# Kernel optimization log

Hardware: AMD Instinct MI355X
Metric: run time of the kernel (lower is better)

## Reference

```python
import jax, jax.numpy as jnp
import numpy as np

N, C_IN, C_OUT, J = 4096, 256, 256, 2
ATT_SLICE = C_OUT * J  # 512
DENSITY = 0.01
NEG_FILL = -1e20


def _sparse_lap(key, n):
    k1, k2 = jax.random.split(key)
    vals = jax.random.normal(k1, (n, n), dtype=jnp.float32)
    mask = jax.random.uniform(k2, (n, n)) < DENSITY
    return vals * mask + jnp.eye(n, dtype=jnp.float32)


def setup_inputs() -> dict:
    key = jax.random.key(0)
    ks = jax.random.split(key, 12)
    s = 0.05
    return {
        "x": jax.random.normal(ks[0], (N, C_IN), dtype=jnp.float32),
        "Lup": _sparse_lap(ks[1], N),
        "Ld": _sparse_lap(ks[2], N),
        "P": _sparse_lap(ks[3], N),
        "Wirr_w": jax.random.normal(ks[4], (J, C_OUT, C_IN), dtype=jnp.float32) * s,
        "Wirr_b": jax.random.normal(ks[5], (J, C_OUT), dtype=jnp.float32) * s,
        "Wsol_w": jax.random.normal(ks[6], (J, C_OUT, C_IN), dtype=jnp.float32) * s,
        "Wsol_b": jax.random.normal(ks[7], (J, C_OUT), dtype=jnp.float32) * s,
        "Whar_w": jax.random.normal(ks[8], (C_OUT, C_IN), dtype=jnp.float32) * s,
        "Whar_b": jax.random.normal(ks[9], (C_OUT,), dtype=jnp.float32) * s,
        "att_irr": jax.random.normal(ks[10], (2 * ATT_SLICE, 1), dtype=jnp.float32) * s,
        "att_sol": jax.random.normal(ks[11], (2 * ATT_SLICE, 1), dtype=jnp.float32) * s,
    }


def _branch(x, L, Ww, Wb, att):
    # x_cat = concat_j(Linear_j(x)) : [N, J*C_OUT]
    x_cat = (jnp.einsum('nc,jdc->njd', x, Ww) + Wb).reshape(x.shape[0], -1)
    src = x_cat @ att[:ATT_SLICE, :]   # [N,1]
    dst = x_cat @ att[ATT_SLICE:, :]   # [N,1]
    E = jax.nn.leaky_relu(src + dst.T, negative_slope=0.01)  # [N,N]
    E = jnp.where(L != 0, E, NEG_FILL)
    alpha = jax.nn.softmax(E, axis=-1)
    z = (alpha @ x) @ Ww[0].T + Wb[0]
    for p in range(1, J):  # Laplacian-power diffusion
        alpha = alpha @ L
        z = z + (alpha @ x) @ Ww[p].T + Wb[p]
    return z


def reference(x, Lup, Ld, P, Wirr_w, Wirr_b, Wsol_w, Wsol_b, Whar_w, Whar_b, att_irr, att_sol):
    z_i = _branch(x, Ld, Wirr_w, Wirr_b, att_irr)
    z_s = _branch(x, Lup, Wsol_w, Wsol_b, att_sol)
    z_har = (P @ x) @ Whar_w.T + Whar_b
    return z_i + z_s + z_har
```

## Files before the change

### kernel.cpp

```cpp
#include <hip/hip_runtime.h>

#define NROW 4096
#define CH   256
#define MAXNNZ 128

typedef short  short8  __attribute__((ext_vector_type(8)));
typedef unsigned short ushort8 __attribute__((ext_vector_type(8)));
typedef float  f32x4   __attribute__((ext_vector_type(4)));

__device__ inline unsigned short f2bf(float f) {
  unsigned u = __float_as_uint(f);
  return (unsigned short)((u + 0x7fffu + ((u >> 16) & 1u)) >> 16);
}
__device__ inline float bf2f(unsigned short h) {
  return __uint_as_float((unsigned)h << 16);
}
__device__ inline int mbcnt64(unsigned long long m, int base) {
  int t = __builtin_amdgcn_mbcnt_lo((unsigned)m, (unsigned)base);
  return __builtin_amdgcn_mbcnt_hi((unsigned)(m >> 32), t);
}

__global__ void cvt_all(const float* __restrict__ x, const float* __restrict__ Wi,
                        const float* __restrict__ Ws, const float* __restrict__ Wh,
                        unsigned short* __restrict__ xbf, unsigned short* __restrict__ Bbf) {
  int i = blockIdx.x * 256 + threadIdx.x;
  const float* src; unsigned short* dst; int o;
  if (i < 262144)        { src = x;  dst = xbf;          o = i; }
  else if (i < 294912)   { src = Wi; dst = Bbf;          o = i - 262144; }
  else if (i < 327680)   { src = Ws; dst = Bbf + 131072; o = i - 294912; }
  else                   { src = Wh; dst = Bbf + 262144; o = i - 327680; }
  float4 v = ((const float4*)src)[o];
  ushort4 u;
  u.x = f2bf(v.x); u.y = f2bf(v.y); u.z = f2bf(v.z); u.w = f2bf(v.w);
  ((ushort4*)dst)[o] = u;
}

__global__ __launch_bounds__(256) void scan_gemm(
    const float* __restrict__ L0, const float* __restrict__ L1,
    const float* __restrict__ L2, int* __restrict__ idx,
    float* __restrict__ val, int* __restrict__ cnt,
    const unsigned short* __restrict__ A, const unsigned short* __restrict__ Bt,
    unsigned short* __restrict__ Y) {
  __shared__ __align__(16) union {
    struct { unsigned short sA[64 * 128]; unsigned short sB[64 * 128]; } g;
    struct { int sj[4][MAXNNZ]; float sv[4][MAXNNZ]; int scnt[4]; } c;
  } u;
  const int bid = blockIdx.x, tid = threadIdx.x;
  const bool is_gemm = (bid < 12800) && (bid % 10 == 9);

  if (is_gemm) {
    const int gid = bid / 10;
    const int m0 = (gid & 63) * 64, n0 = (gid >> 6) * 64;
    const int wid = tid >> 6, lane = tid & 63;
    const int wr = wid >> 1, wc = wid & 1, lr = lane & 15, kg = lane >> 4;
    f32x4 acc[2][2] = {};
#pragma unroll
    for (int kh = 0; kh < 2; ++kh) {
      for (int c = 0; c < 4; ++c) {
        int chunk = c * 256 + tid;
        int r  = chunk >> 4;
        int cb = (chunk & 15) * 16;
        int cbs = cb ^ ((r & 7) << 4);
        ushort8 va = *(const ushort8*)((const char*)A  + (size_t)(m0 + r) * 512 + kh * 256 + cb);
        *(ushort8*)((char*)u.g.sA + r * 256 + cbs) = va;
        ushort8 vb = *(const ushort8*)((const char*)Bt + (size_t)(n0 + r) * 512 + kh * 256 + cb);
        *(ushort8*)((char*)u.g.sB + r * 256 + cbs) = vb;
      }
      __syncthreads();
#pragma unroll
      for (int ks = 0; ks < 4; ++ks) {
        int kb = ks * 64 + kg * 16;
        short8 a0, a1, b0, b1;
        { int r = wr * 32 + lr;      a0 = *(const short8*)((const char*)u.g.sA + r * 256 + (kb ^ ((r & 7) << 4))); }
        { int r = wr * 32 + 16 + lr; a1 = *(const short8*)((const char*)u.g.sA + r * 256 + (kb ^ ((r & 7) << 4))); }
        { int r = wc * 32 + lr;      b0 = *(const short8*)((const char*)u.g.sB + r * 256 + (kb ^ ((r & 7) << 4))); }
        { int r = wc * 32 + 16 + lr; b1 = *(const short8*)((const char*)u.g.sB + r * 256 + (kb ^ ((r & 7) << 4))); }
        acc[0][0] = __builtin_amdgcn_mfma_f32_16x16x32_bf16(a0, b0, acc[0][0], 0, 0, 0);
        acc[0][1] = __builtin_amdgcn_mfma_f32_16x16x32_bf16(a0, b1, acc[0][1], 0, 0, 0);
        acc[1][0] = __builtin_amdgcn_mfma_f32_16x16x32_bf16(a1, b0, acc[1][0], 0, 0, 0);
        acc[1][1] = __builtin_amdgcn_mfma_f32_16x16x32_bf16(a1, b1, acc[1][1], 0, 0, 0);
      }
      __syncthreads();
    }
#pragma unroll
    for (int mi = 0; mi < 2; ++mi)
#pragma unroll
      for (int ni = 0; ni < 2; ++ni) {
        int col = n0 + wc * 32 + ni * 16 + lr;
#pragma unroll
        for (int r4 = 0; r4 < 4; ++r4) {
          int row = m0 + wr * 32 + mi * 16 + kg * 4 + r4;
          Y[(size_t)row * 1280 + col] = f2bf(acc[mi][ni][r4]);
        }
      }
  } else {
    const int cid = bid - ((bid < 12800) ? (bid + 1) / 10 : 1280);
    const int mat = cid >> 12, row = cid & 4095;
    const float* L = (mat == 0) ? L0 : (mat == 1) ? L1 : L2;
    const int wi = tid >> 6, lane = tid & 63;
    const float4* Lseg = (const float4*)(L + (size_t)row * NROW) + wi * 256;

    float4 v0 = Lseg[lane], v1 = Lseg[64 + lane], v2 = Lseg[128 + lane], v3 = Lseg[192 + lane];

    int base = 0;
    float4 vv[4] = {v0, v1, v2, v3};
#pragma unroll
    for (int k = 0; k < 4; ++k) {
      float4 q = vv[k];
      bool n0_ = q.x != 0.f, n1_ = q.y != 0.f, n2_ = q.z != 0.f, n3_ = q.w != 0.f;
      unsigned long long b0 = __ballot(n0_), b1 = __ballot(n1_);
      unsigned long long b2 = __ballot(n2_), b3 = __ballot(n3_);
      int off = mbcnt64(b3, mbcnt64(b2, mbcnt64(b1, mbcnt64(b0, base))));
      int col0 = wi * 1024 + k * 256 + lane * 4;
      if (n0_) { if (off < MAXNNZ) { u.c.sj[wi][off] = col0;     u.c.sv[wi][off] = q.x; } ++off; }
      if (n1_) { if (off < MAXNNZ) { u.c.sj[wi][off] = col0 + 1; u.c.sv[wi][off] = q.y; } ++off; }
      if (n2_) { if (off < MAXNNZ) { u.c.sj[wi][off] = col0 + 2; u.c.sv[wi][off] = q.z; } ++off; }
      if (n3_) { if (off < MAXNNZ) { u.c.sj[wi][off] = col0 + 3; u.c.sv[wi][off] = q.w; } ++off; }
      base += __popcll(b0) + __popcll(b1) + __popcll(b2) + __popcll(b3);
    }
    if (lane == 0) u.c.scnt[wi] = base < MAXNNZ ? base : MAXNNZ;
    __syncthreads();

    int c0 = u.c.scnt[0], c1 = u.c.scnt[1], c2 = u.c.scnt[2], c3 = u.c.scnt[3];
    int total = c0 + c1 + c2 + c3;
    if (total > MAXNNZ) total = MAXNNZ;
    size_t rbase = ((size_t)mat * NROW + row) * MAXNNZ;
    int t = tid;
    if (t < total) {
      int s, o;
      if      (t < c0)           { s = 0; o = t; }
      else if (t < c0 + c1)      { s = 1; o = t - c0; }
      else if (t < c0 + c1 + c2) { s = 2; o = t - c0 - c1; }
      else                       { s = 3; o = t - c0 - c1 - c2; }
      idx[rbase + t] = u.c.sj[s][o];
      val[rbase + t] = u.c.sv[s][o];
    }
    if (t == 0) cnt[mat * NROW + row] = total;
  }
}

__global__ __launch_bounds__(256) void spmm_sdv(
    const int* __restrict__ idx, const float* __restrict__ val,
    const int* __restrict__ cnt, const float* __restrict__ ai,
    const float* __restrict__ as_, const float* __restrict__ bi,
    const float* __restrict__ bs, unsigned short* __restrict__ Y,
    float* __restrict__ sdv) {
  int row = blockIdx.x, t = threadIdx.x, w = t >> 6, l = t & 63;
  __shared__ float satt[2048];
  __shared__ float red2[8];
  __shared__ float sbias[4];
  __shared__ int   sj0[MAXNNZ], sj1[MAXNNZ];
  __shared__ float sv0[MAXNNZ], sv1[MAXNNZ];
  __shared__ float part[4][256];

  for (int k = t; k < 1024; k += 256) { satt[k] = ai[k]; satt[1024 + k] = as_[k]; }
  {
    const float* av = (w & 2) ? as_ : ai;
    const float* bv = (w & 2) ? bs : bi;
    int off = (w & 1) * 512;
    float b = 0.f;
    for (int k = l; k < 512; k += 64) b += av[off + k] * bv[k];
    for (int o = 32; o; o >>= 1) b += __shfl_xor(b, o);
    if (l == 0) sbias[w] = b;
  }
  int n0 = cnt[row], n1 = cnt[NROW + row];
  if (t < n0) { sj0[t] = idx[(size_t)row * MAXNNZ + t];          sv0[t] = val[(size_t)row * MAXNNZ + t]; }
  if (t < n1) { sj1[t] = idx[((size_t)NROW + row) * MAXNNZ + t]; sv1[t] = val[((size_t)NROW + row) * MAXNNZ + t]; }
  ushort4 y4 = *(const ushort4*)(Y + (size_t)row * 1280 + 4 * t);
  __syncthreads();

  {
    int c0 = 4 * t;
    int aoff = (t < 128) ? 0 : 1024;
    int cc = c0 & 511;
    float sp = satt[aoff + cc]       * bf2f(y4.x) + satt[aoff + cc + 1]       * bf2f(y4.y)
             + satt[aoff + cc + 2]   * bf2f(y4.z) + satt[aoff + cc + 3]       * bf2f(y4.w);
    float dp = satt[aoff + 512 + cc] * bf2f(y4.x) + satt[aoff + 512 + cc + 1] * bf2f(y4.y)
             + satt[aoff + 512 + cc + 2] * bf2f(y4.z) + satt[aoff + 512 + cc + 3] * bf2f(y4.w);
    for (int o = 32; o; o >>= 1) { sp += __shfl_xor(sp, o); dp += __shfl_xor(dp, o); }
    if (l == 0) { red2[w * 2] = sp; red2[w * 2 + 1] = dp; }
  }

  float4 acc0 = {0.f, 0.f, 0.f, 0.f}, acc1 = {0.f, 0.f, 0.f, 0.f};
  for (int k = w; k < n0; k += 4) {
    ushort4 y = *(const ushort4*)(Y + (size_t)sj0[k] * 1280 + 256 + 4 * l);
    float a = sv0[k];
    acc0.x += a * bf2f(y.x); acc0.y += a * bf2f(y.y);
    acc0.z += a * bf2f(y.z); acc0.w += a * bf2f(y.w);
  }
  for (int k = w; k < n1; k += 4) {
    ushort4 y = *(const ushort4*)(Y + (size_t)sj1[k] * 1280 + 768 + 4 * l);
    float a = sv1[k];
    acc1.x += a * bf2f(y.x); acc1.y += a * bf2f(y.y);
    acc1.z += a * bf2f(y.z); acc1.w += a * bf2f(y.w);
  }
  ((float4*)part[w])[l] = acc0;
  __syncthreads();
  if (t == 0) {
    sdv[row]            = red2[0] + red2[2] + sbias[0];
    sdv[NROW + row]     = red2[1] + red2[3] + sbias[1];
    sdv[2 * NROW + row] = red2[4] + red2[6] + sbias[2];
    sdv[3 * NROW + row] = red2[5] + red2[7] + sbias[3];
  }
  if (t < 64) {
    unsigned short* yp = Y + (size_t)row * 1280 + 4 * t;
    ushort4 yb = *(const ushort4*)yp;
    ushort4 o;
    o.x = f2bf(bf2f(yb.x) + part[0][4 * t]     + part[1][4 * t]     + part[2][4 * t]     + part[3][4 * t]);
    o.y = f2bf(bf2f(yb.y) + part[0][4 * t + 1] + part[1][4 * t + 1] + part[2][4 * t + 1] + part[3][4 * t + 1]);
    o.z = f2bf(bf2f(yb.z) + part[0][4 * t + 2] + part[1][4 * t + 2] + part[2][4 * t + 2] + part[3][4 * t + 2]);
    o.w = f2bf(bf2f(yb.w) + part[0][4 * t + 3] + part[1][4 * t + 3] + part[2][4 * t + 3] + part[3][4 * t + 3]);
    *(ushort4*)yp = o;
  }
  __syncthreads();
  ((float4*)part[w])[l] = acc1;
  __syncthreads();
  if (t < 64) {
    unsigned short* yp = Y + (size_t)row * 1280 + 512 + 4 * t;
    ushort4 yb = *(const ushort4*)yp;
    ushort4 o;
    o.x = f2bf(bf2f(yb.x) + part[0][4 * t]     + part[1][4 * t]     + part[2][4 * t]     + part[3][4 * t]);
    o.y = f2bf(bf2f(yb.y) + part[0][4 * t + 1] + part[1][4 * t + 1] + part[2][4 * t + 1] + part[3][4 * t + 1]);
    o.z = f2bf(bf2f(yb.z) + part[0][4 * t + 2] + part[1][4 * t + 2] + part[2][4 * t + 2] + part[3][4 * t + 2]);
    o.w = f2bf(bf2f(yb.w) + part[0][4 * t + 3] + part[1][4 * t + 3] + part[2][4 * t + 3] + part[3][4 * t + 3]);
    *(ushort4*)yp = o;
  }
}

__global__ __launch_bounds__(256) void final_z(const int* __restrict__ idx,
                        const float* __restrict__ val, const int* __restrict__ cnt,
                        const float* __restrict__ sdv,
                        const unsigned short* __restrict__ Y,
                        const float* __restrict__ bi, const float* __restrict__ bs,
                        const float* __restrict__ bh, float* __restrict__ Z) {
  int row = blockIdx.x, t = threadIdx.x, w = t >> 6, l = t & 63;
  __shared__ float sa[MAXNNZ];
  __shared__ int   sj[MAXNNZ];
  __shared__ float red[4];
  __shared__ float part[4][256];
  float4 acc = {0.f, 0.f, 0.f, 0.f};

  for (int br = 0; br < 2; ++br) {
    size_t rbase = ((size_t)br * NROW + row) * MAXNNZ;
    int n = cnt[br * NROW + row];
    const float* srcv = sdv + (2 * br) * NROW;
    const float* dstv = sdv + (2 * br + 1) * NROW;
    float e = -1e30f;
    if (t < n) {
      int j = idx[rbase + t];
      sj[t] = j;
      float v = srcv[row] + dstv[j];
      e = v >= 0.f ? v : 0.01f * v;
    }
    float m = e;
    for (int o = 32; o; o >>= 1) m = fmaxf(m, __shfl_xor(m, o));
    if ((t & 63) == 0) red[t >> 6] = m;
    __syncthreads();
    m = fmaxf(fmaxf(red[0], red[1]), fmaxf(red[2], red[3]));
    __syncthreads();
    float p = (t < n) ? expf(e - m) : 0.f;
    float s = p;
    for (int o = 32; o; o >>= 1) s += __shfl_xor(s, o);
    if ((t & 63) == 0) red[t >> 6] = s;
    __syncthreads();
    s = red[0] + red[1] + red[2] + red[3];
    if (t < n) sa[t] = p / s;
    __syncthreads();
    int cd = br ? 512 : 0;
    for (int k = w; k < n; k += 4) {
      ushort4 y = *(const ushort4*)(Y + (size_t)sj[k] * 1280 + cd + 4 * l);
      float a = sa[k];
      acc.x += a * bf2f(y.x); acc.y += a * bf2f(y.y);
      acc.z += a * bf2f(y.z); acc.w += a * bf2f(y.w);
    }
    __syncthreads();
  }

  {
    size_t rbase = ((size_t)2 * NROW + row) * MAXNNZ;
    int n = cnt[2 * NROW + row];
    if (t < n) { sj[t] = idx[rbase + t]; sa[t] = val[rbase + t]; }
    __syncthreads();
    for (int k = w; k < n; k += 4) {
      ushort4 y = *(const ushort4*)(Y + (size_t)sj[k] * 1280 + 1024 + 4 * l);
      float a = sa[k];
      acc.x += a * bf2f(y.x); acc.y += a * bf2f(y.y);
      acc.z += a * bf2f(y.z); acc.w += a * bf2f(y.w);
    }
  }
  ((float4*)part[w])[l] = acc;
  __syncthreads();
  if (t < 64) {
    float4 r;
    int c = 4 * t;
    r.x = part[0][c]     + part[1][c]     + part[2][c]     + part[3][c]     + bi[c]     + bi[256 + c] + bs[c]     + bs[256 + c] + bh[c];
    r.y = part[0][c + 1] + part[1][c + 1] + part[2][c + 1] + part[3][c + 1] + bi[c + 1] + bi[257 + c] + bs[c + 1] + bs[257 + c] + bh[c + 1];
    r.z = part[0][c + 2] + part[1][c + 2] + part[2][c + 2] + part[3][c + 2] + bi[c + 2] + bi[258 + c] + bs[c + 2] + bs[258 + c] + bh[c + 2];
    r.w = part[0][c + 3] + part[1][c + 3] + part[2][c + 3] + part[3][c + 3] + bi[c + 3] + bi[259 + c] + bs[c + 3] + bs[259 + c] + bh[c + 3];
    *(float4*)(Z + (size_t)row * 256 + c) = r;
  }
}

extern "C" void kernel_launch(void* const* d_in, const int* in_sizes, int n_in,
                              void* d_out, int out_size, void* d_ws, size_t ws_size,
                              hipStream_t stream) {
  const float* x      = (const float*)d_in[0];
  const float* Lup    = (const float*)d_in[1];
  const float* Ld     = (const float*)d_in[2];
  const float* P      = (const float*)d_in[3];
  const float* Wirr_w = (const float*)d_in[4];
  const float* Wirr_b = (const float*)d_in[5];
  const float* Wsol_w = (const float*)d_in[6];
  const float* Wsol_b = (const float*)d_in[7];
  const float* Whar_w = (const float*)d_in[8];
  const float* Whar_b = (const float*)d_in[9];
  const float* att_i  = (const float*)d_in[10];
  const float* att_s  = (const float*)d_in[11];
  float* Z = (float*)d_out;

  char* w = (char*)d_ws;
  auto alloc = [&](size_t bytes) { void* p = (void*)w; w += (bytes + 255) & ~(size_t)255; return p; };

  int*   idx  = (int*)alloc((size_t)3 * NROW * MAXNNZ * 4);
  float* val  = (float*)alloc((size_t)3 * NROW * MAXNNZ * 4);
  int*   cnt  = (int*)alloc((size_t)3 * NROW * 4);
  float* sdv  = (float*)alloc(4 * NROW * 4);
  unsigned short* xbf = (unsigned short*)alloc((size_t)NROW * CH * 2);
  unsigned short* Bbf = (unsigned short*)alloc((size_t)1280 * CH * 2);
  unsigned short* Y   = (unsigned short*)alloc((size_t)NROW * 1280 * 2);

  cvt_all<<<(262144 + 32768 + 32768 + 16384) / 256, 256, 0, stream>>>(x, Wirr_w, Wsol_w, Whar_w, xbf, Bbf);

  scan_gemm<<<13568, 256, 0, stream>>>(Ld, Lup, P, idx, val, cnt, xbf, Bbf, Y);

  spmm_sdv<<<NROW, 256, 0, stream>>>(idx, val, cnt, att_i, att_s, Wirr_b, Wsol_b, Y, sdv);

  final_z<<<NROW, 256, 0, stream>>>(idx, val, cnt, sdv, Y, Wirr_b, Wsol_b, Whar_b, Z);
}
```

Measured before the change: 107.8 us.

## Move P-matrix scan into SpMM kernel to overlap with sparse gather work

The CSR compaction scan of the third dense matrix (P) moves out of the combined scan+GEMM kernel and into the SpMM/score kernel. Even blocks scan rows of P while odd blocks do the SpMM, sharing LDS through a union. The GEMM-interleave ratio in the first kernel is retuned to 1 in 7 to fit the smaller scan grid. The aim is to balance memory-bound dense scanning against the latency-bound gather SpMM so the two overlap, instead of leaving the SpMM kernel short of bandwidth-heavy work. The cost is a larger second grid and branch-divergent block roles.

Measured after the change: 122.7 us. 13.9% more time.

```diff
diff --git a/kernel.cpp b/kernel.cpp
--- a/kernel.cpp
+++ b/kernel.cpp
@@ -37,8 +37,7 @@
 
 __global__ __launch_bounds__(256) void scan_gemm(
     const float* __restrict__ L0, const float* __restrict__ L1,
-    const float* __restrict__ L2, int* __restrict__ idx,
-    float* __restrict__ val, int* __restrict__ cnt,
+    int* __restrict__ idx, float* __restrict__ val, int* __restrict__ cnt,
     const unsigned short* __restrict__ A, const unsigned short* __restrict__ Bt,
     unsigned short* __restrict__ Y) {
   __shared__ __align__(16) union {
@@ -46,10 +45,10 @@
     struct { int sj[4][MAXNNZ]; float sv[4][MAXNNZ]; int scnt[4]; } c;
   } u;
   const int bid = blockIdx.x, tid = threadIdx.x;
-  const bool is_gemm = (bid < 12800) && (bid % 10 == 9);
+  const bool is_gemm = (bid < 8960) && (bid % 7 == 6);
 
   if (is_gemm) {
-    const int gid = bid / 10;
+    const int gid = bid / 7;
     const int m0 = (gid & 63) * 64, n0 = (gid >> 6) * 64;
     const int wid = tid >> 6, lane = tid & 63;
     const int wr = wid >> 1, wc = wid & 1, lr = lane & 15, kg = lane >> 4;
@@ -94,9 +93,9 @@
         }
       }
   } else {
-    const int cid = bid - ((bid < 12800) ? (bid + 1) / 10 : 1280);
+    const int cid = (bid < 8960) ? (bid - (bid + 1) / 7) : (bid - 1280);
     const int mat = cid >> 12, row = cid & 4095;
-    const float* L = (mat == 0) ? L0 : (mat == 1) ? L1 : L2;
+    const float* L = (mat == 0) ? L0 : L1;
     const int wi = tid >> 6, lane = tid & 63;
     const float4* Lseg = (const float4*)(L + (size_t)row * NROW) + wi * 256;
 
@@ -139,91 +138,134 @@
   }
 }
 
-__global__ __launch_bounds__(256) void spmm_sdv(
-    const int* __restrict__ idx, const float* __restrict__ val,
-    const int* __restrict__ cnt, const float* __restrict__ ai,
-    const float* __restrict__ as_, const float* __restrict__ bi,
-    const float* __restrict__ bs, unsigned short* __restrict__ Y,
-    float* __restrict__ sdv) {
-  int row = blockIdx.x, t = threadIdx.x, w = t >> 6, l = t & 63;
-  __shared__ float satt[2048];
-  __shared__ float red2[8];
-  __shared__ float sbias[4];
-  __shared__ int   sj0[MAXNNZ], sj1[MAXNNZ];
-  __shared__ float sv0[MAXNNZ], sv1[MAXNNZ];
-  __shared__ float part[4][256];
-
-  for (int k = t; k < 1024; k += 256) { satt[k] = ai[k]; satt[1024 + k] = as_[k]; }
-  {
-    const float* av = (w & 2) ? as_ : ai;
-    const float* bv = (w & 2) ? bs : bi;
-    int off = (w & 1) * 512;
-    float b = 0.f;
-    for (int k = l; k < 512; k += 64) b += av[off + k] * bv[k];
-    for (int o = 32; o; o >>= 1) b += __shfl_xor(b, o);
-    if (l == 0) sbias[w] = b;
-  }
-  int n0 = cnt[row], n1 = cnt[NROW + row];
-  if (t < n0) { sj0[t] = idx[(size_t)row * MAXNNZ + t];          sv0[t] = val[(size_t)row * MAXNNZ + t]; }
-  if (t < n1) { sj1[t] = idx[((size_t)NROW + row) * MAXNNZ + t]; sv1[t] = val[((size_t)NROW + row) * MAXNNZ + t]; }
-  ushort4 y4 = *(const ushort4*)(Y + (size_t)row * 1280 + 4 * t);
-  __syncthreads();
-
-  {
-    int c0 = 4 * t;
-    int aoff = (t < 128) ? 0 : 1024;
-    int cc = c0 & 511;
-    float sp = satt[aoff + cc]       * bf2f(y4.x) + satt[aoff + cc + 1]       * bf2f(y4.y)
-             + satt[aoff + cc + 2]   * bf2f(y4.z) + satt[aoff + cc + 3]       * bf2f(y4.w);
-    float dp = satt[aoff + 512 + cc] * bf2f(y4.x) + satt[aoff + 512 + cc + 1] * bf2f(y4.y)
-             + satt[aoff + 512 + cc + 2] * bf2f(y4.z) + satt[aoff + 512 + cc + 3] * bf2f(y4.w);
-    for (int o = 32; o; o >>= 1) { sp += __shfl_xor(sp, o); dp += __shfl_xor(dp, o); }
-    if (l == 0) { red2[w * 2] = sp; red2[w * 2 + 1] = dp; }
-  }
-
-  float4 acc0 = {0.f, 0.f, 0.f, 0.f}, acc1 = {0.f, 0.f, 0.f, 0.f};
-  for (int k = w; k < n0; k += 4) {
-    ushort4 y = *(const ushort4*)(Y + (size_t)sj0[k] * 1280 + 256 + 4 * l);
-    float a = sv0[k];
-    acc0.x += a * bf2f(y.x); acc0.y += a * bf2f(y.y);
-    acc0.z += a * bf2f(y.z); acc0.w += a * bf2f(y.w);
-  }
-  for (int k = w; k < n1; k += 4) {
-    ushort4 y = *(const ushort4*)(Y + (size_t)sj1[k] * 1280 + 768 + 4 * l);
-    float a = sv1[k];
-    acc1.x += a * bf2f(y.x); acc1.y += a * bf2f(y.y);
-    acc1.z += a * bf2f(y.z); acc1.w += a * bf2f(y.w);
-  }
-  ((float4*)part[w])[l] = acc0;
-  __syncthreads();
-  if (t == 0) {
-    sdv[row]            = red2[0] + red2[2] + sbias[0];
-    sdv[NROW + row]     = red2[1] + red2[3] + sbias[1];
-    sdv[2 * NROW + row] = red2[4] + red2[6] + sbias[2];
-    sdv[3 * NROW + row] = red2[5] + red2[7] + sbias[3];
-  }
-  if (t < 64) {
-    unsigned short* yp = Y + (size_t)row * 1280 + 4 * t;
-    ushort4 yb = *(const ushort4*)yp;
-    ushort4 o;
-    o.x = f2bf(bf2f(yb.x) + part[0][4 * t]     + part[1][4 * t]     + part[2][4 * t]     + part[3][4 * t]);
-    o.y = f2bf(bf2f(yb.y) + part[0][4 * t + 1] + part[1][4 * t + 1] + part[2][4 * t + 1] + part[3][4 * t + 1]);
-    o.z = f2bf(bf2f(yb.z) + part[0][4 * t + 2] + part[1][4 * t + 2] + part[2][4 * t + 2] + part[3][4 * t + 2]);
-    o.w = f2bf(bf2f(yb.w) + part[0][4 * t + 3] + part[1][4 * t + 3] + part[2][4 * t + 3] + part[3][4 * t + 3]);
-    *(ushort4*)yp = o;
-  }
-  __syncthreads();
-  ((float4*)part[w])[l] = acc1;
-  __syncthreads();
-  if (t < 64) {
-    unsigned short* yp = Y + (size_t)row * 1280 + 512 + 4 * t;
-    ushort4 yb = *(const ushort4*)yp;
-    ushort4 o;
-    o.x = f2bf(bf2f(yb.x) + part[0][4 * t]     + part[1][4 * t]     + part[2][4 * t]     + part[3][4 * t]);
-    o.y = f2bf(bf2f(yb.y) + part[0][4 * t + 1] + part[1][4 * t + 1] + part[2][4 * t + 1] + part[3][4 * t + 1]);
-    o.z = f2bf(bf2f(yb.z) + part[0][4 * t + 2] + part[1][4 * t + 2] + part[2][4 * t + 2] + part[3][4 * t + 2]);
-    o.w = f2bf(bf2f(yb.w) + part[0][4 * t + 3] + part[1][4 * t + 3] + part[2][4 * t + 3] + part[3][4 * t + 3]);
-    *(ushort4*)yp = o;
+__global__ __launch_bounds__(256) void scan_spmm(
+    const float* __restrict__ L2, int* __restrict__ idx,
+    float* __restrict__ val, int* __restrict__ cnt,
+    const float* __restrict__ ai, const float* __restrict__ as_,
+    const float* __restrict__ bi, const float* __restrict__ bs,
+    unsigned short* __restrict__ Y, float* __restrict__ sdv) {
+  __shared__ __align__(16) union {
+    struct { int sj[4][MAXNNZ]; float sv[4][MAXNNZ]; int scnt[4]; } c;
+    struct {
+      float satt[2048]; float red2[8]; float sbias[4];
+      int sj0[MAXNNZ]; int sj1[MAXNNZ]; float sv0[MAXNNZ]; float sv1[MAXNNZ];
+      float part[4][256];
+    } s;
+  } u;
+  const int bid = blockIdx.x, tid = threadIdx.x;
+  const int row = bid >> 1;
+  const int w = tid >> 6, l = tid & 63;
+
+  if ((bid & 1) == 0) {
+    const float4* Lseg = (const float4*)(L2 + (size_t)row * NROW) + w * 256;
+    float4 v0 = Lseg[l], v1 = Lseg[64 + l], v2 = Lseg[128 + l], v3 = Lseg[192 + l];
+    int base = 0;
+    float4 vv[4] = {v0, v1, v2, v3};
+#pragma unroll
+    for (int k = 0; k < 4; ++k) {
+      float4 q = vv[k];
+      bool n0_ = q.x != 0.f, n1_ = q.y != 0.f, n2_ = q.z != 0.f, n3_ = q.w != 0.f;
+      unsigned long long b0 = __ballot(n0_), b1 = __ballot(n1_);
+      unsigned long long b2 = __ballot(n2_), b3 = __ballot(n3_);
+      int off = mbcnt64(b3, mbcnt64(b2, mbcnt64(b1, mbcnt64(b0, base))));
+      int col0 = w * 1024 + k * 256 + l * 4;
+      if (n0_) { if (off < MAXNNZ) { u.c.sj[w][off] = col0;     u.c.sv[w][off] = q.x; } ++off; }
+      if (n1_) { if (off < MAXNNZ) { u.c.sj[w][off] = col0 + 1; u.c.sv[w][off] = q.y; } ++off; }
+      if (n2_) { if (off < MAXNNZ) { u.c.sj[w][off] = col0 + 2; u.c.sv[w][off] = q.z; } ++off; }
+      if (n3_) { if (off < MAXNNZ) { u.c.sj[w][off] = col0 + 3; u.c.sv[w][off] = q.w; } ++off; }
+      base += __popcll(b0) + __popcll(b1) + __popcll(b2) + __popcll(b3);
+    }
+    if (l == 0) u.c.scnt[w] = base < MAXNNZ ? base : MAXNNZ;
+    __syncthreads();
+    int c0 = u.c.scnt[0], c1 = u.c.scnt[1], c2 = u.c.scnt[2], c3 = u.c.scnt[3];
+    int total = c0 + c1 + c2 + c3;
+    if (total > MAXNNZ) total = MAXNNZ;
+    size_t rbase = ((size_t)2 * NROW + row) * MAXNNZ;
+    int t = tid;
+    if (t < total) {
+      int s, o;
+      if      (t < c0)           { s = 0; o = t; }
+      else if (t < c0 + c1)      { s = 1; o = t - c0; }
+      else if (t < c0 + c1 + c2) { s = 2; o = t - c0 - c1; }
+      else                       { s = 3; o = t - c0 - c1 - c2; }
+      idx[rbase + t] = u.c.sj[s][o];
+      val[rbase + t] = u.c.sv[s][o];
+    }
+    if (t == 0) cnt[2 * NROW + row] = total;
+  } else {
+    int t = tid;
+    for (int k = t; k < 1024; k += 256) { u.s.satt[k] = ai[k]; u.s.satt[1024 + k] = as_[k]; }
+    {
+      const float* av = (w & 2) ? as_ : ai;
+      const float* bv = (w & 2) ? bs : bi;
+      int off = (w & 1) * 512;
+      float b = 0.f;
+      for (int k = l; k < 512; k += 64) b += av[off + k] * bv[k];
+      for (int o = 32; o; o >>= 1) b += __shfl_xor(b, o);
+      if (l == 0) u.s.sbias[w] = b;
+    }
+    int n0 = cnt[row], n1 = cnt[NROW + row];
+    if (t < n0) { u.s.sj0[t] = idx[(size_t)row * MAXNNZ + t];          u.s.sv0[t] = val[(size_t)row * MAXNNZ + t]; }
+    if (t < n1) { u.s.sj1[t] = idx[((size_t)NROW + row) * MAXNNZ + t]; u.s.sv1[t] = val[((size_t)NROW + row) * MAXNNZ + t]; }
+    ushort4 y4 = *(const ushort4*)(Y + (size_t)row * 1280 + 4 * t);
+    __syncthreads();
+
+    {
+      int c0 = 4 * t;
+      int aoff = (t < 128) ? 0 : 1024;
+      int cc = c0 & 511;
+      float sp = u.s.satt[aoff + cc]       * bf2f(y4.x) + u.s.satt[aoff + cc + 1]       * bf2f(y4.y)
+               + u.s.satt[aoff + cc + 2]   * bf2f(y4.z) + u.s.satt[aoff + cc + 3]       * bf2f(y4.w);
+      float dp = u.s.satt[aoff + 512 + cc] * bf2f(y4.x) + u.s.satt[aoff + 512 + cc + 1] * bf2f(y4.y)
+               + u.s.satt[aoff + 512 + cc + 2] * bf2f(y4.z) + u.s.satt[aoff + 512 + cc + 3] * bf2f(y4.w);
+      for (int o = 32; o; o >>= 1) { sp += __shfl_xor(sp, o); dp += __shfl_xor(dp, o); }
+      if (l == 0) { u.s.red2[w * 2] = sp; u.s.red2[w * 2 + 1] = dp; }
+    }
+
+    float4 acc0 = {0.f, 0.f, 0.f, 0.f}, acc1 = {0.f, 0.f, 0.f, 0.f};
+    for (int k = w; k < n0; k += 4) {
+      ushort4 y = *(const ushort4*)(Y + (size_t)u.s.sj0[k] * 1280 + 256 + 4 * l);
+      float a = u.s.sv0[k];
+      acc0.x += a * bf2f(y.x); acc0.y += a * bf2f(y.y);
+      acc0.z += a * bf2f(y.z); acc0.w += a * bf2f(y.w);
+    }
+    for (int k = w; k < n1; k += 4) {
+      ushort4 y = *(const ushort4*)(Y + (size_t)u.s.sj1[k] * 1280 + 768 + 4 * l);
+      float a = u.s.sv1[k];
+      acc1.x += a * bf2f(y.x); acc1.y += a * bf2f(y.y);
+      acc1.z += a * bf2f(y.z); acc1.w += a * bf2f(y.w);
+    }
+    ((float4*)u.s.part[w])[l] = acc0;
+    __syncthreads();
+    if (t == 0) {
+      sdv[row]            = u.s.red2[0] + u.s.red2[2] + u.s.sbias[0];
+      sdv[NROW + row]     = u.s.red2[1] + u.s.red2[3] + u.s.sbias[1];
+      sdv[2 * NROW + row] = u.s.red2[4] + u.s.red2[6] + u.s.sbias[2];
+      sdv[3 * NROW + row] = u.s.red2[5] + u.s.red2[7] + u.s.sbias[3];
+    }
+    if (t < 64) {
+      unsigned short* yp = Y + (size_t)row * 1280 + 4 * t;
+      ushort4 yb = *(const ushort4*)yp;
+      ushort4 o;
+      o.x = f2bf(bf2f(yb.x) + u.s.part[0][4 * t]     + u.s.part[1][4 * t]     + u.s.part[2][4 * t]     + u.s.part[3][4 * t]);
+      o.y = f2bf(bf2f(yb.y) + u.s.part[0][4 * t + 1] + u.s.part[1][4 * t + 1] + u.s.part[2][4 * t + 1] + u.s.part[3][4 * t + 1]);
+      o.z = f2bf(bf2f(yb.z) + u.s.part[0][4 * t + 2] + u.s.part[1][4 * t + 2] + u.s.part[2][4 * t + 2] + u.s.part[3][4 * t + 2]);
+      o.w = f2bf(bf2f(yb.w) + u.s.part[0][4 * t + 3] + u.s.part[1][4 * t + 3] + u.s.part[2][4 * t + 3] + u.s.part[3][4 * t + 3]);
+      *(ushort4*)yp = o;
+    }
+    __syncthreads();
+    ((float4*)u.s.part[w])[l] = acc1;
+    __syncthreads();
+    if (t < 64) {
+      unsigned short* yp = Y + (size_t)row * 1280 + 512 + 4 * t;
+      ushort4 yb = *(const ushort4*)yp;
+      ushort4 o;
+      o.x = f2bf(bf2f(yb.x) + u.s.part[0][4 * t]     + u.s.part[1][4 * t]     + u.s.part[2][4 * t]     + u.s.part[3][4 * t]);
+      o.y = f2bf(bf2f(yb.y) + u.s.part[0][4 * t + 1] + u.s.part[1][4 * t + 1] + u.s.part[2][4 * t + 1] + u.s.part[3][4 * t + 1]);
+      o.z = f2bf(bf2f(yb.z) + u.s.part[0][4 * t + 2] + u.s.part[1][4 * t + 2] + u.s.part[2][4 * t + 2] + u.s.part[3][4 * t + 2]);
+      o.w = f2bf(bf2f(yb.w) + u.s.part[0][4 * t + 3] + u.s.part[1][4 * t + 3] + u.s.part[2][4 * t + 3] + u.s.part[3][4 * t + 3]);
+      *(ushort4*)yp = o;
+    }
   }
 }
 
@@ -331,9 +373,9 @@
 
   cvt_all<<<(262144 + 32768 + 32768 + 16384) / 256, 256, 0, stream>>>(x, Wirr_w, Wsol_w, Whar_w, xbf, Bbf);
 
-  scan_gemm<<<13568, 256, 0, stream>>>(Ld, Lup, P, idx, val, cnt, xbf, Bbf, Y);
-
-  spmm_sdv<<<NROW, 256, 0, stream>>>(idx, val, cnt, att_i, att_s, Wirr_b, Wsol_b, Y, sdv);
+  scan_gemm<<<9472, 256, 0, stream>>>(Ld, Lup, idx, val, cnt, xbf, Bbf, Y);
+
+  scan_spmm<<<8192, 256, 0, stream>>>(P, idx, val, cnt, att_i, att_s, Wirr_b, Wsol_b, Y, sdv);
 
   final_z<<<NROW, 256, 0, stream>>>(idx, val, cnt, sdv, Y, Wirr_b, Wsol_b, Whar_b, Z);
 }
```
